# Kernel tuning notes

Measured on AMD Instinct MI355X. Metric: run time of the kernel, lower is better.

## Reference

```python
import jax, jax.numpy as jnp
import numpy as np
import math

N_CHANNELS = 256
D_K = 64
N_HEADS = N_CHANNELS // D_K  # 4
N_GROUPS = 32
EPS = 1e-5
SCALE = 1.0 / math.sqrt(math.sqrt(D_K))


def setup_inputs() -> dict:
    key = jax.random.key(0)
    ks = jax.random.split(key, 7)
    B, C, H, W = 2, N_CHANNELS, 64, 64
    inner = N_HEADS * D_K
    x = jax.random.normal(ks[0], (B, C, H, W), dtype=jnp.float32)
    gn_w = jnp.ones((C,), dtype=jnp.float32)
    gn_b = jnp.zeros((C,), dtype=jnp.float32)
    proj_w = jax.random.normal(ks[1], (3 * inner, C), dtype=jnp.float32) / math.sqrt(C)
    proj_b = jnp.zeros((3 * inner,), dtype=jnp.float32)
    out_w = jax.random.normal(ks[2], (C, inner), dtype=jnp.float32) / math.sqrt(inner)
    out_b = jnp.zeros((C,), dtype=jnp.float32)
    return {"x": x, "gn_w": gn_w, "gn_b": gn_b, "proj_w": proj_w,
            "proj_b": proj_b, "out_w": out_w, "out_b": out_b}


def _group_norm(x, gamma, beta):
    # x: [B, C, H, W], 32 groups, affine per channel
    B, C, H, W = x.shape
    xg = x.reshape(B, N_GROUPS, C // N_GROUPS, H * W)
    mean = xg.mean(axis=(2, 3), keepdims=True)
    var = xg.var(axis=(2, 3), keepdims=True)
    xn = (xg - mean) * jax.lax.rsqrt(var + EPS)
    xn = xn.reshape(B, C, H, W)
    return xn * gamma[None, :, None, None] + beta[None, :, None, None]


def reference(x, gn_w, gn_b, proj_w, proj_b, out_w, out_b):
    B, C, H, W = x.shape
    S = H * W
    h = _group_norm(x, gn_w, gn_b).reshape(B, C, S).transpose(0, 2, 1)  # [B, S, C]
    qkv = h @ proj_w.T + proj_b                                          # [B, S, 3*nh*dk]
    qkv = qkv.reshape(B, S, N_HEADS, 3 * D_K)
    q, k, v = jnp.split(qkv, 3, axis=-1)                                 # [B, S, nh, dk] each
    # bihd,bjhd->bijh with scale applied to both q and k (net 1/sqrt(dk))
    attn = jnp.einsum('bihd,bjhd->bijh', q * SCALE, k * SCALE)
    attn = jax.nn.softmax(attn, axis=2)
    res = jnp.einsum('bijh,bjhd->bihd', attn, v).reshape(B, S, N_HEADS * D_K)
    res = res @ out_w.T + out_b                                          # [B, S, C]
    res = res.transpose(0, 2, 1).reshape(B, C, H, W)
    return res + x
```

## Files before the change

kernel.cpp:

```cpp
#include <hip/hip_runtime.h>
#include <math.h>

#define NB 2
#define NC 256
#define NS 4096
#define NG 32
#define CPG 8
#define NH 4
#define DK 64
#define NQKV 768
#define NKG 4
#define TPG 16
#define QS 0.18033688011112042f

typedef __attribute__((ext_vector_type(8))) short short8;
typedef __attribute__((ext_vector_type(4))) float f32x4;
typedef __attribute__((ext_vector_type(16))) float f32x16;
typedef __attribute__((ext_vector_type(4))) unsigned uint4v;

union U8 { uint4v u; short8 s; };

__device__ __forceinline__ short f2bf(float f){
  union { float f; unsigned u; } v; v.f = f;
  unsigned r = v.u + 0x7fffu + ((v.u >> 16) & 1u);
  return (short)(r >> 16);
}
__device__ __forceinline__ float ex2(float x){
  float y; asm("v_exp_f32 %0, %1" : "=v"(y) : "v"(x)); return y;
}
__device__ __forceinline__ unsigned cvtpk(float lo, float hi){
  unsigned u; asm("v_cvt_pk_bf16_f32 %0, %1, %2" : "=v"(u) : "v"(lo), "v"(hi)); return u;
}
__device__ __forceinline__ void pl32swap(unsigned &x, unsigned &y){
  asm("v_permlane32_swap_b32 %0, %1" : "+v"(x), "+v"(y));
}

__global__ __launch_bounds__(256) void k_stats(const float* __restrict__ x,
                                               float* __restrict__ sbuf){
  int blk = blockIdx.x;
  int bg = blk >> 2, qt = blk & 3;
  const float* base = x + (size_t)bg*(CPG*NS) + (size_t)qt*(CPG*NS/4);
  const f32x4* b4 = (const f32x4*)base;
  float s = 0.f, ss = 0.f;
  #pragma unroll
  for (int it = 0; it < 8; ++it){
    f32x4 v = b4[it*256 + threadIdx.x];
    s  += (v[0]+v[1])+(v[2]+v[3]);
    ss += (v[0]*v[0]+v[1]*v[1])+(v[2]*v[2]+v[3]*v[3]);
  }
  for (int o = 32; o > 0; o >>= 1){ s += __shfl_down(s,o); ss += __shfl_down(ss,o); }
  __shared__ float red[8];
  int w = threadIdx.x >> 6;
  if ((threadIdx.x & 63) == 0){ red[w] = s; red[4+w] = ss; }
  __syncthreads();
  if (threadIdx.x == 0){
    float S  = red[0]+red[1]+red[2]+red[3];
    float SS = red[4]+red[5]+red[6]+red[7];
    atomicAdd(&sbuf[bg], S);
    atomicAdd(&sbuf[64 + bg], SS);
  }
}

__global__ __launch_bounds__(256) void k_apply(const float* __restrict__ x,
                                               const float* __restrict__ sbuf,
                                               const float* __restrict__ gw,
                                               const float* __restrict__ gb,
                                               const float* __restrict__ pw,
                                               const float* __restrict__ ow,
                                               short* __restrict__ h,
                                               short* __restrict__ pwb,
                                               short* __restrict__ owb){
  int blk = blockIdx.x;
  int tid = threadIdx.x;
  if (blk < 256){
    int bg = blk >> 2, qt = blk & 3;
    int b = bg >> 5, g = bg & 31;
    const float* base = x + (size_t)bg*(CPG*NS);
    const float inv = 1.f/(float)(CPG*NS);
    float mu = sbuf[bg]*inv;
    float rs = rsqrtf(sbuf[64+bg]*inv - mu*mu + 1e-5f);
    float wv[8], bv[8];
    #pragma unroll
    for (int c = 0; c < 8; ++c){
      wv[c] = gw[g*8 + c] * rs;
      bv[c] = gb[g*8 + c] - mu * wv[c];
    }
    short* hb = h + (size_t)b*NS*NC + g*8;
    int s0 = qt << 10;
    #pragma unroll
    for (int it = 0; it < 4; ++it){
      int i = s0 + it*256 + tid;
      unsigned u[4];
      #pragma unroll
      for (int c2 = 0; c2 < 4; ++c2){
        float v0 = base[(size_t)(2*c2  )*NS + i]*wv[2*c2  ] + bv[2*c2  ];
        float v1 = base[(size_t)(2*c2+1)*NS + i]*wv[2*c2+1] + bv[2*c2+1];
        u[c2] = cvtpk(v0, v1);
      }
      *(uint4v*)&hb[(size_t)i*NC] = (uint4v){u[0],u[1],u[2],u[3]};
    }
  } else {
    int i = (blk - 256)*256 + tid;
    if (i < NQKV*NC) pwb[i] = f2bf(pw[i]);
    if (i < NC*NC)   owb[i] = f2bf(ow[i]);
  }
}

__global__ __launch_bounds__(256) void k_qkv(const short* __restrict__ h,
                                             const short* __restrict__ wb,
                                             const float* __restrict__ pb,
                                             short* __restrict__ qo,
                                             short* __restrict__ ko,
                                             short* __restrict__ vto){
  __shared__ short As[64][72];
  __shared__ short Bs[128][72];
  int m0 = blockIdx.x << 6;
  int n0 = blockIdx.y << 7;
  int tid = threadIdx.x;
  int lane = tid & 63, wid = tid >> 6;
  int wm = (wid >> 1) << 5, wn = (wid & 1) << 6;
  int l15 = lane & 15, lg = lane >> 4;
  const f32x4 fz = {0.f,0.f,0.f,0.f};
  f32x4 acc[2][4];
  for (int i=0;i<2;i++) for(int j=0;j<4;j++) acc[i][j] = fz;
  for (int k0 = 0; k0 < NC; k0 += 64){
    __syncthreads();
    for (int it = 0; it < 2; ++it){
      int c = it*256 + tid;
      int r = c >> 3, ch = (c & 7) << 3;
      *(short8*)&As[r][ch] = *(const short8*)&h[((size_t)(m0 + r))*NC + k0 + ch];
    }
    for (int it = 0; it < 4; ++it){
      int c = it*256 + tid;
      int r = c >> 3, ch = (c & 7) << 3;
      *(short8*)&Bs[r][ch] = *(const short8*)&wb[((size_t)(n0 + r))*NC + k0 + ch];
    }
    __syncthreads();
    #pragma unroll
    for (int kk = 0; kk < 2; ++kk){
      short8 a[2], b[4];
      for (int mf=0; mf<2; ++mf) a[mf] = *(const short8*)&As[wm + mf*16 + l15][kk*32 + lg*8];
      for (int nf=0; nf<4; ++nf) b[nf] = *(const short8*)&Bs[wn + nf*16 + l15][kk*32 + lg*8];
      for (int mf=0; mf<2; ++mf)
        for (int nf=0; nf<4; ++nf)
          acc[mf][nf] = __builtin_amdgcn_mfma_f32_16x16x32_bf16(a[mf], b[nf], acc[mf][nf], 0,0,0);
    }
  }
  for (int mf=0; mf<2; ++mf)
    for (int nf=0; nf<4; ++nf)
      for (int r=0; r<4; ++r){
        int m = m0 + wm + mf*16 + lg*4 + r;
        int o = n0 + wn + nf*16 + l15;
        float val = acc[mf][nf][r] + pb[o];
        int b_ = m >> 12, s = m & 4095;
        int hh = o / 192, rem = o - hh*192;
        int t = rem >> 6, d = rem & 63;
        size_t bh = (size_t)(b_*NH + hh);
        if (t == 0)      qo [(bh*NS + s)*DK + d] = f2bf(val * QS);
        else if (t == 1) ko [(bh*NS + s)*DK + d] = f2bf(val);
        else             vto[(bh*DK + d)*NS + s] = f2bf(val);
      }
}

struct SMK { short kv[NKG][2][2][64][72]; };
struct SMC {
  float gOB[3][4][64][33];
  float ml[3][4][2][32];
  float fOB[4][64][33];
};

__global__ __launch_bounds__(1024, 4) void k_attn(const short* __restrict__ q,
                                                  const short* __restrict__ k,
                                                  const short* __restrict__ vt,
                                                  short* __restrict__ ao){
  extern __shared__ char smem[];
  SMK* sk = (SMK*)smem;
  SMC* sc = (SMC*)smem;

  int blk = blockIdx.x;
  int bh = blk & 7;
  int q0 = (blk >> 3) << 7;
  const short* Qb = q  + (size_t)bh*NS*DK;
  const short* Kb = k  + (size_t)bh*NS*DK;
  const short* Vb = vt + (size_t)bh*DK*NS;
  int tid = threadIdx.x, lane = tid & 63, wid = tid >> 6;
  int l31 = lane & 31, hi = lane >> 5;
  int g = wid >> 2, wq = wid & 3;
  int gtid = tid & 255;
  int kvbase = g << 10;

  short8 bq[4];
  {
    const short* qrow = Qb + (size_t)(q0 + wq*32 + l31)*DK + hi*8;
    #pragma unroll
    for (int s2 = 0; s2 < 4; ++s2) bq[s2] = *(const short8*)(qrow + s2*16);
  }

  f32x16 ot0, ot1;
  #pragma unroll
  for (int i = 0; i < 16; ++i){ ot0[i] = 0.f; ot1[i] = 0.f; }
  float mrun = -1e30f, lrun = 0.f;

  short8 kpre[2], vpre[2];
  #pragma unroll
  for (int it = 0; it < 2; ++it){
    int c = it*256 + gtid, r = c >> 3, col = (c & 7) << 3;
    kpre[it] = *(const short8*)&Kb[(size_t)(kvbase + r)*DK + col];
    vpre[it] = *(const short8*)&Vb[(size_t)r*NS + kvbase + col];
  }
  #pragma unroll
  for (int it = 0; it < 2; ++it){
    int c = it*256 + gtid, r = c >> 3, col = (c & 7) << 3;
    *(short8*)&sk->kv[g][0][0][r][col] = kpre[it];
    *(short8*)&sk->kv[g][0][1][r][col] = vpre[it];
  }
  #pragma unroll
  for (int it = 0; it < 2; ++it){
    int c = it*256 + gtid, r = c >> 3, col = (c & 7) << 3;
    kpre[it] = *(const short8*)&Kb[(size_t)(kvbase + 64 + r)*DK + col];
    vpre[it] = *(const short8*)&Vb[(size_t)r*NS + kvbase + 64 + col];
  }

  for (int t = 0; t < TPG; ++t){
    __syncthreads();
    const short (*Kl)[72] = sk->kv[g][t & 1][0];
    const short (*Vl)[72] = sk->kv[g][t & 1][1];
    f32x16 st0, st1;
    #pragma unroll
    for (int i = 0; i < 16; ++i){ st0[i] = 0.f; st1[i] = 0.f; }
    const short* Kr0 = &Kl[l31][hi*8];
    const short* Kr1 = &Kl[32 + l31][hi*8];
    #pragma unroll
    for (int s2 = 0; s2 < 4; ++s2){
      short8 ka0 = *(const short8*)(Kr0 + s2*16);
      short8 ka1 = *(const short8*)(Kr1 + s2*16);
      st0 = __builtin_amdgcn_mfma_f32_32x32x16_bf16(ka0, bq[s2], st0, 0,0,0);
      st1 = __builtin_amdgcn_mfma_f32_32x32x16_bf16(ka1, bq[s2], st1, 0,0,0);
    }
    if (t + 1 < TPG){
      int nb = (t + 1) & 1;
      #pragma unroll
      for (int it = 0; it < 2; ++it){
        int c = it*256 + gtid, r = c >> 3, col = (c & 7) << 3;
        *(short8*)&sk->kv[g][nb][0][r][col] = kpre[it];
        *(short8*)&sk->kv[g][nb][1][r][col] = vpre[it];
      }
    }
    if (t + 2 < TPG){
      int kv0 = kvbase + (t + 2)*64;
      #pragma unroll
      for (int it = 0; it < 2; ++it){
        int c = it*256 + gtid, r = c >> 3, col = (c & 7) << 3;
        kpre[it] = *(const short8*)&Kb[(size_t)(kv0 + r)*DK + col];
        vpre[it] = *(const short8*)&Vb[(size_t)r*NS + kv0 + col];
      }
    }
    float mx = -1e30f;
    #pragma unroll
    for (int i = 0; i < 16; ++i) mx = fmaxf(mx, fmaxf(st0[i], st1[i]));
    mx = fmaxf(mx, __shfl_xor(mx, 32));
    if (!__all(mx - mrun <= 8.f)){
      float mnew = fmaxf(mrun, mx);
      float corr = ex2(mrun - mnew);
      lrun *= corr;
      #pragma unroll
      for (int i = 0; i < 16; ++i){ ot0[i] *= corr; ot1[i] *= corr; }
      mrun = mnew;
    }
    float p0[16], p1[16]; float ps = 0.f;
    #pragma unroll
    for (int i = 0; i < 16; ++i){
      p0[i] = ex2(st0[i] - mrun); p1[i] = ex2(st1[i] - mrun);
      ps += p0[i] + p1[i];
    }
    ps += __shfl_xor(ps, 32);
    lrun += ps;
    unsigned pk0[8], pk1[8];
    #pragma unroll
    for (int a = 0; a < 4; ++a){
      pk0[a]     = cvtpk(p0[4*a+0], p0[4*a+1]);
      pk1[a]     = cvtpk(p0[4*a+2], p0[4*a+3]);
      pk0[4 + a] = cvtpk(p1[4*a+0], p1[4*a+1]);
      pk1[4 + a] = cvtpk(p1[4*a+2], p1[4*a+3]);
    }
    const short* Vr0 = &Vl[l31][hi*8];
    const short* Vr1 = &Vl[32 + l31][hi*8];
    #pragma unroll
    for (int i2 = 0; i2 < 4; ++i2){
      unsigned w0 = pk0[2*i2], w2 = pk0[2*i2+1]; pl32swap(w0, w2);
      unsigned w1 = pk1[2*i2], w3 = pk1[2*i2+1]; pl32swap(w1, w3);
      U8 cv; cv.u = (uint4v){w0, w1, w2, w3};
      short8 av0 = *(const short8*)(Vr0 + i2*16);
      short8 av1 = *(const short8*)(Vr1 + i2*16);
      ot0 = __builtin_amdgcn_mfma_f32_32x32x16_bf16(av0, cv.s, ot0, 0,0,0);
      ot1 = __builtin_amdgcn_mfma_f32_32x32x16_bf16(av1, cv.s, ot1, 0,0,0);
    }
  }

  __syncthreads();
  if (g > 0){
    #pragma unroll
    for (int r2 = 0; r2 < 16; ++r2){
      int dl = (r2 & 3) + 8*(r2 >> 2) + 4*hi;
      sc->gOB[g-1][wq][dl][l31]      = ot0[r2];
      sc->gOB[g-1][wq][32 + dl][l31] = ot1[r2];
    }
    if (hi == 0){ sc->ml[g-1][wq][0][l31] = mrun; sc->ml[g-1][wq][1][l31] = lrun; }
  }
  __syncthreads();
  if (g == 0){
    float m1 = sc->ml[0][wq][0][l31], l1 = sc->ml[0][wq][1][l31];
    float m2 = sc->ml[1][wq][0][l31], l2 = sc->ml[1][wq][1][l31];
    float m3 = sc->ml[2][wq][0][l31], l3 = sc->ml[2][wq][1][l31];
    float M  = fmaxf(fmaxf(mrun, m1), fmaxf(m2, m3));
    float w0 = ex2(mrun - M), w1 = ex2(m1 - M), w2 = ex2(m2 - M), w3 = ex2(m3 - M);
    float inv = 1.f/(lrun*w0 + l1*w1 + l2*w2 + l3*w3);
    w0 *= inv; w1 *= inv; w2 *= inv; w3 *= inv;
    #pragma unroll
    for (int r2 = 0; r2 < 16; ++r2){
      int dl = (r2 & 3) + 8*(r2 >> 2) + 4*hi;
      sc->fOB[wq][dl][l31] = ot0[r2]*w0 + sc->gOB[0][wq][dl][l31]*w1
                           + sc->gOB[1][wq][dl][l31]*w2 + sc->gOB[2][wq][dl][l31]*w3;
      sc->fOB[wq][32+dl][l31] = ot1[r2]*w0 + sc->gOB[0][wq][32+dl][l31]*w1
                              + sc->gOB[1][wq][32+dl][l31]*w2 + sc->gOB[2][wq][32+dl][l31]*w3;
    }
  }
  __syncthreads();
  {
    int ql = tid >> 3, dc = (tid & 7) << 3;
    int b_ = bh >> 2, hh = bh & 3;
    float v2[8];
    #pragma unroll
    for (int i = 0; i < 8; ++i) v2[i] = sc->fOB[ql >> 5][dc + i][ql & 31];
    uint4v wa = { cvtpk(v2[0],v2[1]), cvtpk(v2[2],v2[3]),
                  cvtpk(v2[4],v2[5]), cvtpk(v2[6],v2[7]) };
    size_t base = ((size_t)b_*NS + q0 + ql)*NC + hh*DK + dc;
    *(uint4v*)&ao[base] = wa;
  }
}

__global__ __launch_bounds__(256) void k_out(const short* __restrict__ aoin,
                                             const short* __restrict__ wb,
                                             const float* __restrict__ ob,
                                             const float* __restrict__ x,
                                             float* __restrict__ out){
  __shared__ short As[64][40];
  __shared__ short Bs[64][40];
  int m0 = blockIdx.x << 6;
  int n0 = blockIdx.y << 6;
  int tid = threadIdx.x;
  int lane = tid & 63, wid = tid >> 6;
  int wm = (wid >> 1) << 5, wn = (wid & 1) << 5;
  int l15 = lane & 15, lg = lane >> 4;
  const f32x4 fz = {0.f,0.f,0.f,0.f};
  f32x4 acc[2][2];
  for (int i=0;i<2;i++) for(int j=0;j<2;j++) acc[i][j] = fz;
  for (int k0 = 0; k0 < NC; k0 += 32){
    __syncthreads();
    {
      int c = tid;
      int r = c >> 2, kk8 = (c & 3) << 3;
      *(short8*)&As[r][kk8] = *(const short8*)&aoin[((size_t)(m0 + r))*NC + k0 + kk8];
      *(short8*)&Bs[r][kk8] = *(const short8*)&wb  [((size_t)(n0 + r))*NC + k0 + kk8];
    }
    __syncthreads();
    short8 a[2], b[2];
    for (int mf=0; mf<2; ++mf) a[mf] = *(const short8*)&As[wm + mf*16 + l15][lg*8];
    for (int nf=0; nf<2; ++nf) b[nf] = *(const short8*)&Bs[wn + nf*16 + l15][lg*8];
    for (int mf=0; mf<2; ++mf)
      for (int nf=0; nf<2; ++nf)
        acc[mf][nf] = __builtin_amdgcn_mfma_f32_16x16x32_bf16(a[mf], b[nf], acc[mf][nf], 0,0,0);
  }
  for (int mf=0; mf<2; ++mf)
    for (int nf=0; nf<2; ++nf)
      for (int r=0; r<4; ++r){
        int m = m0 + wm + mf*16 + lg*4 + r;
        int o = n0 + wn + nf*16 + l15;
        int b_ = m >> 12, s = m & 4095;
        size_t idx = ((size_t)b_*NC + o)*NS + s;
        out[idx] = acc[mf][nf][r] + ob[o] + x[idx];
      }
}

extern "C" void kernel_launch(void* const* d_in, const int* in_sizes, int n_in,
                              void* d_out, int out_size, void* d_ws, size_t ws_size,
                              hipStream_t stream){
  const float* x   = (const float*)d_in[0];
  const float* gnw = (const float*)d_in[1];
  const float* gnb = (const float*)d_in[2];
  const float* pw  = (const float*)d_in[3];
  const float* pb  = (const float*)d_in[4];
  const float* ow  = (const float*)d_in[5];
  const float* ob  = (const float*)d_in[6];
  float* out = (float*)d_out;

  char* ws = (char*)d_ws;
  float* sbuf = (float*)ws;
  short* wqkv = (short*)(ws + 512);
  short* wout = wqkv + NQKV*NC;
  short* h    = wout + NC*NC;
  short* qb   = h   + (size_t)NB*NS*NC;
  short* kb   = qb  + (size_t)NB*NH*NS*DK;
  short* vtb  = kb  + (size_t)NB*NH*NS*DK;
  short* ao   = vtb + (size_t)NB*NH*NS*DK;

  hipMemsetAsync(sbuf, 0, 512, stream);
  k_stats<<<256, 256, 0, stream>>>(x, sbuf);
  k_apply<<<1024, 256, 0, stream>>>(x, sbuf, gnw, gnb, pw, ow, h, wqkv, wout);
  k_qkv<<<dim3(128, 6), 256, 0, stream>>>(h, wqkv, pb, qb, kb, vtb);
  k_attn<<<256, 1024, sizeof(SMK), stream>>>(qb, kb, vtb, ao);
  k_out<<<dim3(128, 4), 256, 0, stream>>>(ao, wout, ob, x, out);
}
```

Measured before the change: 89.93 us.

## Load K/V fragments directly from global memory in attention, dropping LDS staging

```diff
diff --git a/kernel.cpp b/kernel.cpp
--- a/kernel.cpp
+++ b/kernel.cpp
@@ -162,7 +162,6 @@
       }
 }
 
-struct SMK { short kv[NKG][2][2][64][72]; };
 struct SMC {
   float gOB[3][4][64][33];
   float ml[3][4][2][32];
@@ -174,7 +173,6 @@
                                                   const short* __restrict__ vt,
                                                   short* __restrict__ ao){
   extern __shared__ char smem[];
-  SMK* sk = (SMK*)smem;
   SMC* sc = (SMC*)smem;
 
   int blk = blockIdx.x;
@@ -186,7 +184,6 @@
   int tid = threadIdx.x, lane = tid & 63, wid = tid >> 6;
   int l31 = lane & 31, hi = lane >> 5;
   int g = wid >> 2, wq = wid & 3;
-  int gtid = tid & 255;
   int kvbase = g << 10;
 
   short8 bq[4];
@@ -201,59 +198,25 @@
   for (int i = 0; i < 16; ++i){ ot0[i] = 0.f; ot1[i] = 0.f; }
   float mrun = -1e30f, lrun = 0.f;
 
-  short8 kpre[2], vpre[2];
-  #pragma unroll
-  for (int it = 0; it < 2; ++it){
-    int c = it*256 + gtid, r = c >> 3, col = (c & 7) << 3;
-    kpre[it] = *(const short8*)&Kb[(size_t)(kvbase + r)*DK + col];
-    vpre[it] = *(const short8*)&Vb[(size_t)r*NS + kvbase + col];
-  }
-  #pragma unroll
-  for (int it = 0; it < 2; ++it){
-    int c = it*256 + gtid, r = c >> 3, col = (c & 7) << 3;
-    *(short8*)&sk->kv[g][0][0][r][col] = kpre[it];
-    *(short8*)&sk->kv[g][0][1][r][col] = vpre[it];
-  }
-  #pragma unroll
-  for (int it = 0; it < 2; ++it){
-    int c = it*256 + gtid, r = c >> 3, col = (c & 7) << 3;
-    kpre[it] = *(const short8*)&Kb[(size_t)(kvbase + 64 + r)*DK + col];
-    vpre[it] = *(const short8*)&Vb[(size_t)r*NS + kvbase + 64 + col];
-  }
+  const short* Kp0 = Kb + (size_t)(kvbase + l31)*DK + hi*8;
+  const short* Kp1 = Kp0 + 32*DK;
+  const short* Vp0 = Vb + (size_t)l31*NS + kvbase + hi*8;
+  const short* Vp1 = Vp0 + (size_t)32*NS;
 
   for (int t = 0; t < TPG; ++t){
-    __syncthreads();
-    const short (*Kl)[72] = sk->kv[g][t & 1][0];
-    const short (*Vl)[72] = sk->kv[g][t & 1][1];
+    short8 ka0[4], ka1[4];
+    #pragma unroll
+    for (int s2 = 0; s2 < 4; ++s2){
+      ka0[s2] = *(const short8*)(Kp0 + s2*16);
+      ka1[s2] = *(const short8*)(Kp1 + s2*16);
+    }
     f32x16 st0, st1;
     #pragma unroll
     for (int i = 0; i < 16; ++i){ st0[i] = 0.f; st1[i] = 0.f; }
-    const short* Kr0 = &Kl[l31][hi*8];
-    const short* Kr1 = &Kl[32 + l31][hi*8];
     #pragma unroll
     for (int s2 = 0; s2 < 4; ++s2){
-      short8 ka0 = *(const short8*)(Kr0 + s2*16);
-      short8 ka1 = *(const short8*)(Kr1 + s2*16);
-      st0 = __builtin_amdgcn_mfma_f32_32x32x16_bf16(ka0, bq[s2], st0, 0,0,0);
-      st1 = __builtin_amdgcn_mfma_f32_32x32x16_bf16(ka1, bq[s2], st1, 0,0,0);
-    }
-    if (t + 1 < TPG){
-      int nb = (t + 1) & 1;
-      #pragma unroll
-      for (int it = 0; it < 2; ++it){
-        int c = it*256 + gtid, r = c >> 3, col = (c & 7) << 3;
-        *(short8*)&sk->kv[g][nb][0][r][col] = kpre[it];
-        *(short8*)&sk->kv[g][nb][1][r][col] = vpre[it];
-      }
-    }
-    if (t + 2 < TPG){
-      int kv0 = kvbase + (t + 2)*64;
-      #pragma unroll
-      for (int it = 0; it < 2; ++it){
-        int c = it*256 + gtid, r = c >> 3, col = (c & 7) << 3;
-        kpre[it] = *(const short8*)&Kb[(size_t)(kv0 + r)*DK + col];
-        vpre[it] = *(const short8*)&Vb[(size_t)r*NS + kv0 + col];
-      }
+      st0 = __builtin_amdgcn_mfma_f32_32x32x16_bf16(ka0[s2], bq[s2], st0, 0,0,0);
+      st1 = __builtin_amdgcn_mfma_f32_32x32x16_bf16(ka1[s2], bq[s2], st1, 0,0,0);
     }
     float mx = -1e30f;
     #pragma unroll
@@ -283,18 +246,18 @@
       pk0[4 + a] = cvtpk(p1[4*a+0], p1[4*a+1]);
       pk1[4 + a] = cvtpk(p1[4*a+2], p1[4*a+3]);
     }
-    const short* Vr0 = &Vl[l31][hi*8];
-    const short* Vr1 = &Vl[32 + l31][hi*8];
     #pragma unroll
     for (int i2 = 0; i2 < 4; ++i2){
+      short8 av0 = *(const short8*)(Vp0 + i2*16);
+      short8 av1 = *(const short8*)(Vp1 + i2*16);
       unsigned w0 = pk0[2*i2], w2 = pk0[2*i2+1]; pl32swap(w0, w2);
       unsigned w1 = pk1[2*i2], w3 = pk1[2*i2+1]; pl32swap(w1, w3);
       U8 cv; cv.u = (uint4v){w0, w1, w2, w3};
-      short8 av0 = *(const short8*)(Vr0 + i2*16);
-      short8 av1 = *(const short8*)(Vr1 + i2*16);
       ot0 = __builtin_amdgcn_mfma_f32_32x32x16_bf16(av0, cv.s, ot0, 0,0,0);
       ot1 = __builtin_amdgcn_mfma_f32_32x32x16_bf16(av1, cv.s, ot1, 0,0,0);
     }
+    Kp0 += 64*DK; Kp1 += 64*DK;
+    Vp0 += 64;    Vp1 += 64;
   }
 
   __syncthreads();
@@ -408,6 +371,6 @@
   k_stats<<<256, 256, 0, stream>>>(x, sbuf);
   k_apply<<<1024, 256, 0, stream>>>(x, sbuf, gnw, gnb, pw, ow, h, wqkv, wout);
   k_qkv<<<dim3(128, 6), 256, 0, stream>>>(h, wqkv, pb, qb, kb, vtb);
-  k_attn<<<256, 1024, sizeof(SMK), stream>>>(qb, kb, vtb, ao);
+  k_attn<<<256, 1024, sizeof(SMC), stream>>>(qb, kb, vtb, ao);
   k_out<<<dim3(128, 4), 256, 0, stream>>>(ao, wout, ob, x, out);
 }
```

Measured after the change: 160.9 us. 1.79x slower.
